# Performance work log

Hardware: AMD Instinct MI355X
Metric: run time of the kernel (lower is better)

The kernel has to match this reference:

```python
import jax, jax.numpy as jnp
import numpy as np

B, T_ENC, ENC, DEC, MEL = 32, 1024, 1024, 1024, 80


def setup_inputs() -> dict:
    key = jax.random.key(0)
    ks = jax.random.split(key, 10)
    s = lambda k, shape, sc=1.0: (jax.random.normal(k, shape, dtype=jnp.float32) * sc)
    return {
        "prev_mel_frame": s(ks[0], (B, MEL)),
        "encoder_outputs": s(ks[1], (B, T_ENC, ENC)),
        "h": s(ks[2], (B, DEC)),
        "c": s(ks[3], (B, DEC)),
        # AdditiveAttention learned scale vector (use_scale=True default)
        "attn_scale": s(ks[4], (ENC,), 0.05),
        # LSTMCell params: input dim = MEL + ENC, gates order i, f, c, o (Keras)
        "kernel": s(ks[5], (MEL + ENC, 4 * DEC), 0.02),
        "rec_kernel": s(ks[6], (DEC, 4 * DEC), 0.02),
        "bias": s(ks[7], (4 * DEC,), 0.02),
        # Dense projection to mel
        "proj_w": s(ks[8], (DEC, MEL), 0.02),
        "proj_b": s(ks[9], (MEL,), 0.02),
    }


def reference(prev_mel_frame, encoder_outputs, h, c,
              attn_scale, kernel, rec_kernel, bias, proj_w, proj_b):
    # Additive (Bahdanau) attention: scores[b,t] = sum_d scale_d * tanh(h[b,d] + enc[b,t,d])
    feat = jnp.tanh(h[:, None, :] + encoder_outputs)          # [B, T, D]
    scores = jnp.einsum("btd,d->bt", feat, attn_scale)         # [B, T]
    attn = jax.nn.softmax(scores, axis=-1)
    context = jnp.einsum("bt,btd->bd", attn, encoder_outputs)  # [B, ENC]

    # LSTMCell step on concat([prev_mel, context])
    x = jnp.concatenate([prev_mel_frame, context], axis=-1)    # [B, MEL+ENC]
    z = x @ kernel + h @ rec_kernel + bias                     # [B, 4*DEC]
    i, f, g, o = jnp.split(z, 4, axis=-1)
    i = jax.nn.sigmoid(i)
    f = jax.nn.sigmoid(f)
    o = jax.nn.sigmoid(o)
    c_new = f * c + i * jnp.tanh(g)
    h_new = o * jnp.tanh(c_new)

    mel_frame = h_new @ proj_w + proj_b                        # [B, MEL]
    return mel_frame, h_new, c_new
```

## Files before the change

kernel.cpp:

```cpp
#include <hip/hip_runtime.h>

#define BB 32
#define TT 1024
#define ENCD 1024
#define DECD 1024
#define MELD 80
#define KTOT (MELD + ENCD + DECD)
#define NZ (4 * DECD)
#define KCH 64
#define KC 34
#define NTT 32

__device__ float g_scores[BB * TT];
__device__ float g_cp[NTT * BB * ENCD];
__device__ float g_ctx[BB * ENCD];
__device__ float g_zp[KC * BB * NZ];
__device__ float g_hn[BB * DECD];

__device__ __forceinline__ float tanh_fast(float x) {
    return 1.f - __fdividef(2.f, __expf(2.f * x) + 1.f);
}
__device__ __forceinline__ float sigmoid_fast(float x) {
    return __fdividef(1.f, 1.f + __expf(-x));
}

__global__ __launch_bounds__(256) void k_scores(const float* __restrict__ enc,
                                                const float* __restrict__ h,
                                                const float* __restrict__ scale) {
    int w = blockIdx.x * 4 + (threadIdx.x >> 6);
    int lane = threadIdx.x & 63;
    int b = w >> 10;
    const float4* ep = (const float4*)(enc + (size_t)w * ENCD);
    const float4* hp = (const float4*)(h + (size_t)b * DECD);
    const float4* sp = (const float4*)scale;
    float sum = 0.f;
#pragma unroll
    for (int j = 0; j < 4; j++) {
        int i = lane + j * 64;
        float4 e = ep[i], hv = hp[i], s = sp[i];
        sum += s.x * tanh_fast(hv.x + e.x);
        sum += s.y * tanh_fast(hv.y + e.y);
        sum += s.z * tanh_fast(hv.z + e.z);
        sum += s.w * tanh_fast(hv.w + e.w);
    }
#pragma unroll
    for (int off = 32; off > 0; off >>= 1) sum += __shfl_down(sum, off, 64);
    if (lane == 0) g_scores[w] = sum;
}

__global__ __launch_bounds__(256) void k_context(const float* __restrict__ enc) {
    int b = blockIdx.x, tt = blockIdx.y, tid = threadIdx.x;
    __shared__ float red[4];
    __shared__ float la[32];
    float v[4];
#pragma unroll
    for (int i = 0; i < 4; i++) v[i] = g_scores[b * TT + tid + i * 256];
    float m = fmaxf(fmaxf(v[0], v[1]), fmaxf(v[2], v[3]));
#pragma unroll
    for (int off = 32; off > 0; off >>= 1) m = fmaxf(m, __shfl_down(m, off, 64));
    if ((tid & 63) == 0) red[tid >> 6] = m;
    __syncthreads();
    m = fmaxf(fmaxf(red[0], red[1]), fmaxf(red[2], red[3]));
    __syncthreads();
    float s = 0.f;
#pragma unroll
    for (int i = 0; i < 4; i++) s += __expf(v[i] - m);
#pragma unroll
    for (int off = 32; off > 0; off >>= 1) s += __shfl_down(s, off, 64);
    if ((tid & 63) == 0) red[tid >> 6] = s;
    __syncthreads();
    s = red[0] + red[1] + red[2] + red[3];
    float inv = __fdividef(1.f, s);
    if (tid < 32) la[tid] = __expf(g_scores[b * TT + tt * 32 + tid] - m) * inv;
    __syncthreads();

    const float4* ep = (const float4*)(enc + ((size_t)b * TT + tt * 32) * ENCD) + tid;
    float ax = 0.f, ay = 0.f, az = 0.f, aw = 0.f;
#pragma unroll 8
    for (int t = 0; t < 32; t++) {
        float4 e = ep[(size_t)t * (ENCD / 4)];
        float w = la[t];
        ax = fmaf(w, e.x, ax); ay = fmaf(w, e.y, ay);
        az = fmaf(w, e.z, az); aw = fmaf(w, e.w, aw);
    }
    float4 r; r.x = ax; r.y = ay; r.z = az; r.w = aw;
    ((float4*)g_cp)[((size_t)tt * BB + b) * (ENCD / 4) + tid] = r;
}

__global__ __launch_bounds__(256) void k_ctxsum() {
    int i = blockIdx.x * 256 + threadIdx.x;
    float a = 0.f;
#pragma unroll 8
    for (int tt = 0; tt < NTT; tt++) a += g_cp[tt * (BB * ENCD) + i];
    g_ctx[i] = a;
}

__global__ __launch_bounds__(256) void k_zmm(const float* __restrict__ pm,
                                             const float* __restrict__ h,
                                             const float* __restrict__ kern,
                                             const float* __restrict__ reck) {
    __shared__ float xs[KCH * 32];
    int jt = blockIdx.x & 15, kc = blockIdx.x >> 4;
    int k0 = kc * KCH;
    int kcount = min(KCH, KTOT - k0);
    int tid = threadIdx.x;
    for (int idx = tid; idx < kcount * 32; idx += 256) {
        int kk = idx >> 5, b = idx & 31;
        int k = k0 + kk;
        float v;
        if (k < MELD)             v = pm[b * MELD + k];
        else if (k < MELD + ENCD) v = g_ctx[b * ENCD + (k - MELD)];
        else                      v = h[b * DECD + (k - MELD - ENCD)];
        xs[idx] = v;
    }
    __syncthreads();
    int j = jt * 256 + tid;
    float acc[32];
#pragma unroll
    for (int b = 0; b < 32; b++) acc[b] = 0.f;
    for (int kk0 = 0; kk0 < kcount; kk0 += 8) {
        float w[8];
#pragma unroll
        for (int i = 0; i < 8; i++) {
            int k = k0 + kk0 + i;
            w[i] = (k < MELD + ENCD) ? kern[(size_t)k * NZ + j]
                                     : reck[(size_t)(k - MELD - ENCD) * NZ + j];
        }
#pragma unroll
        for (int i = 0; i < 8; i++) {
            const float* xr = xs + (kk0 + i) * 32;
#pragma unroll
            for (int b = 0; b < 32; b++) acc[b] = fmaf(xr[b], w[i], acc[b]);
        }
    }
#pragma unroll
    for (int b = 0; b < 32; b++) g_zp[((size_t)kc * BB + b) * NZ + j] = acc[b];
}

__global__ __launch_bounds__(256) void k_gates(const float* __restrict__ bias,
                                               const float* __restrict__ c,
                                               float* __restrict__ out) {
    __shared__ float sacc[4][4][64];
    int b = blockIdx.x >> 4, jq = blockIdx.x & 15;
    int jl = threadIdx.x & 63, grp = threadIdx.x >> 6;
    int j = jq * 64 + jl;
    int kc0 = grp * 9;
    int kc1 = min(kc0 + 9, KC);
    float zi = 0.f, zf = 0.f, zg = 0.f, zo = 0.f;
    for (int kc = kc0; kc < kc1; kc++) {
        const float* zp = g_zp + ((size_t)kc * BB + b) * NZ;
        zi += zp[j];
        zf += zp[1024 + j];
        zg += zp[2048 + j];
        zo += zp[3072 + j];
    }
    sacc[grp][0][jl] = zi; sacc[grp][1][jl] = zf;
    sacc[grp][2][jl] = zg; sacc[grp][3][jl] = zo;
    __syncthreads();
    if (grp == 0) {
        zi = sacc[0][0][jl] + sacc[1][0][jl] + sacc[2][0][jl] + sacc[3][0][jl] + bias[j];
        zf = sacc[0][1][jl] + sacc[1][1][jl] + sacc[2][1][jl] + sacc[3][1][jl] + bias[1024 + j];
        zg = sacc[0][2][jl] + sacc[1][2][jl] + sacc[2][2][jl] + sacc[3][2][jl] + bias[2048 + j];
        zo = sacc[0][3][jl] + sacc[1][3][jl] + sacc[2][3][jl] + sacc[3][3][jl] + bias[3072 + j];
        int idx = b * 1024 + j;
        float cn = sigmoid_fast(zf) * c[idx] + sigmoid_fast(zi) * tanh_fast(zg);
        float hn = sigmoid_fast(zo) * tanh_fast(cn);
        g_hn[idx] = hn;
        out[2560 + idx] = hn;
        out[35328 + idx] = cn;
    }
}

__global__ __launch_bounds__(256) void k_proj(const float* __restrict__ pw,
                                              const float* __restrict__ pb,
                                              float* __restrict__ out) {
    __shared__ float lh[1024];
    __shared__ float pacc[2][MELD];
    int b = blockIdx.x, tid = threadIdx.x;
    for (int i = tid; i < 1024; i += 256) lh[i] = g_hn[b * 1024 + i];
    __syncthreads();
    int m = tid & 127;
    int g = tid >> 7;
    if (m < MELD) {
        float acc = 0.f;
        int d0 = g * 512;
#pragma unroll 8
        for (int d = d0; d < d0 + 512; d++) acc = fmaf(lh[d], pw[d * MELD + m], acc);
        pacc[g][m] = acc;
    }
    __syncthreads();
    if (tid < MELD) out[b * MELD + tid] = pacc[0][tid] + pacc[1][tid] + pb[tid];
}

extern "C" void kernel_launch(void* const* d_in, const int* in_sizes, int n_in,
                              void* d_out, int out_size, void* d_ws, size_t ws_size,
                              hipStream_t stream) {
    const float* pm   = (const float*)d_in[0];
    const float* enc  = (const float*)d_in[1];
    const float* h    = (const float*)d_in[2];
    const float* c    = (const float*)d_in[3];
    const float* asc  = (const float*)d_in[4];
    const float* kern = (const float*)d_in[5];
    const float* reck = (const float*)d_in[6];
    const float* bias = (const float*)d_in[7];
    const float* pw   = (const float*)d_in[8];
    const float* pb   = (const float*)d_in[9];
    float* out = (float*)d_out;

    k_scores <<<8192, 256, 0, stream>>>(enc, h, asc);
    k_context<<<dim3(32, NTT), 256, 0, stream>>>(enc);
    k_ctxsum <<<128, 256, 0, stream>>>();
    k_zmm    <<<544, 256, 0, stream>>>(pm, h, kern, reck);
    k_gates  <<<512, 256, 0, stream>>>(bias, c, out);
    k_proj   <<<32, 256, 0, stream>>>(pw, pb, out);
}
```

Before: 299.5 us.

## Fuse attention scores, softmax and context into one online-softmax pass

```diff
diff --git a/kernel.cpp b/kernel.cpp
--- a/kernel.cpp
+++ b/kernel.cpp
@@ -11,8 +11,9 @@
 #define KC 34
 #define NTT 32
 
-__device__ float g_scores[BB * TT];
 __device__ float g_cp[NTT * BB * ENCD];
+__device__ float g_m[NTT * BB];
+__device__ float g_s[NTT * BB];
 __device__ float g_ctx[BB * ENCD];
 __device__ float g_zp[KC * BB * NZ];
 __device__ float g_hn[BB * DECD];
@@ -24,75 +25,122 @@
     return __fdividef(1.f, 1.f + __expf(-x));
 }
 
-__global__ __launch_bounds__(256) void k_scores(const float* __restrict__ enc,
-                                                const float* __restrict__ h,
-                                                const float* __restrict__ scale) {
-    int w = blockIdx.x * 4 + (threadIdx.x >> 6);
-    int lane = threadIdx.x & 63;
-    int b = w >> 10;
-    const float4* ep = (const float4*)(enc + (size_t)w * ENCD);
-    const float4* hp = (const float4*)(h + (size_t)b * DECD);
+__global__ __launch_bounds__(256) void k_attn(const float* __restrict__ enc,
+                                              const float* __restrict__ hst,
+                                              const float* __restrict__ scale) {
+    int b = blockIdx.x, tc = blockIdx.y;
+    int w = threadIdx.x >> 6, lane = threadIdx.x & 63;
+    const float4* hp = (const float4*)(hst + (size_t)b * DECD);
     const float4* sp = (const float4*)scale;
-    float sum = 0.f;
-#pragma unroll
-    for (int j = 0; j < 4; j++) {
-        int i = lane + j * 64;
-        float4 e = ep[i], hv = hp[i], s = sp[i];
-        sum += s.x * tanh_fast(hv.x + e.x);
-        sum += s.y * tanh_fast(hv.y + e.y);
-        sum += s.z * tanh_fast(hv.z + e.z);
-        sum += s.w * tanh_fast(hv.w + e.w);
-    }
-#pragma unroll
-    for (int off = 32; off > 0; off >>= 1) sum += __shfl_down(sum, off, 64);
-    if (lane == 0) g_scores[w] = sum;
-}
-
-__global__ __launch_bounds__(256) void k_context(const float* __restrict__ enc) {
-    int b = blockIdx.x, tt = blockIdx.y, tid = threadIdx.x;
-    __shared__ float red[4];
-    __shared__ float la[32];
-    float v[4];
-#pragma unroll
-    for (int i = 0; i < 4; i++) v[i] = g_scores[b * TT + tid + i * 256];
-    float m = fmaxf(fmaxf(v[0], v[1]), fmaxf(v[2], v[3]));
-#pragma unroll
-    for (int off = 32; off > 0; off >>= 1) m = fmaxf(m, __shfl_down(m, off, 64));
-    if ((tid & 63) == 0) red[tid >> 6] = m;
-    __syncthreads();
-    m = fmaxf(fmaxf(red[0], red[1]), fmaxf(red[2], red[3]));
-    __syncthreads();
-    float s = 0.f;
-#pragma unroll
-    for (int i = 0; i < 4; i++) s += __expf(v[i] - m);
-#pragma unroll
-    for (int off = 32; off > 0; off >>= 1) s += __shfl_down(s, off, 64);
-    if ((tid & 63) == 0) red[tid >> 6] = s;
-    __syncthreads();
-    s = red[0] + red[1] + red[2] + red[3];
-    float inv = __fdividef(1.f, s);
-    if (tid < 32) la[tid] = __expf(g_scores[b * TT + tt * 32 + tid] - m) * inv;
-    __syncthreads();
-
-    const float4* ep = (const float4*)(enc + ((size_t)b * TT + tt * 32) * ENCD) + tid;
+    float4 hr0 = hp[lane], hr1 = hp[lane + 64], hr2 = hp[lane + 128], hr3 = hp[lane + 192];
+    float4 sr0 = sp[lane], sr1 = sp[lane + 64], sr2 = sp[lane + 128], sr3 = sp[lane + 192];
+
+    float m = -1e30f, s = 0.f;
+    float4 c0 = {0.f, 0.f, 0.f, 0.f}, c1 = c0, c2 = c0, c3 = c0;
+
+    const float4* ep = (const float4*)(enc + ((size_t)b * TT + tc * 32 + w * 8) * ENCD) + lane;
+#pragma unroll 2
+    for (int t = 0; t < 8; t++) {
+        float4 e0 = ep[t * 256];
+        float4 e1 = ep[t * 256 + 64];
+        float4 e2 = ep[t * 256 + 128];
+        float4 e3 = ep[t * 256 + 192];
+        float sc = 0.f;
+        sc = fmaf(sr0.x, tanh_fast(hr0.x + e0.x), sc);
+        sc = fmaf(sr0.y, tanh_fast(hr0.y + e0.y), sc);
+        sc = fmaf(sr0.z, tanh_fast(hr0.z + e0.z), sc);
+        sc = fmaf(sr0.w, tanh_fast(hr0.w + e0.w), sc);
+        sc = fmaf(sr1.x, tanh_fast(hr1.x + e1.x), sc);
+        sc = fmaf(sr1.y, tanh_fast(hr1.y + e1.y), sc);
+        sc = fmaf(sr1.z, tanh_fast(hr1.z + e1.z), sc);
+        sc = fmaf(sr1.w, tanh_fast(hr1.w + e1.w), sc);
+        sc = fmaf(sr2.x, tanh_fast(hr2.x + e2.x), sc);
+        sc = fmaf(sr2.y, tanh_fast(hr2.y + e2.y), sc);
+        sc = fmaf(sr2.z, tanh_fast(hr2.z + e2.z), sc);
+        sc = fmaf(sr2.w, tanh_fast(hr2.w + e2.w), sc);
+        sc = fmaf(sr3.x, tanh_fast(hr3.x + e3.x), sc);
+        sc = fmaf(sr3.y, tanh_fast(hr3.y + e3.y), sc);
+        sc = fmaf(sr3.z, tanh_fast(hr3.z + e3.z), sc);
+        sc = fmaf(sr3.w, tanh_fast(hr3.w + e3.w), sc);
+#pragma unroll
+        for (int off = 32; off; off >>= 1) sc += __shfl_xor(sc, off, 64);
+        if (sc > m) {
+            float al = __expf(m - sc);
+            s = fmaf(s, al, 1.f);
+            c0.x = fmaf(c0.x, al, e0.x); c0.y = fmaf(c0.y, al, e0.y);
+            c0.z = fmaf(c0.z, al, e0.z); c0.w = fmaf(c0.w, al, e0.w);
+            c1.x = fmaf(c1.x, al, e1.x); c1.y = fmaf(c1.y, al, e1.y);
+            c1.z = fmaf(c1.z, al, e1.z); c1.w = fmaf(c1.w, al, e1.w);
+            c2.x = fmaf(c2.x, al, e2.x); c2.y = fmaf(c2.y, al, e2.y);
+            c2.z = fmaf(c2.z, al, e2.z); c2.w = fmaf(c2.w, al, e2.w);
+            c3.x = fmaf(c3.x, al, e3.x); c3.y = fmaf(c3.y, al, e3.y);
+            c3.z = fmaf(c3.z, al, e3.z); c3.w = fmaf(c3.w, al, e3.w);
+            m = sc;
+        } else {
+            float p = __expf(sc - m);
+            s += p;
+            c0.x = fmaf(p, e0.x, c0.x); c0.y = fmaf(p, e0.y, c0.y);
+            c0.z = fmaf(p, e0.z, c0.z); c0.w = fmaf(p, e0.w, c0.w);
+            c1.x = fmaf(p, e1.x, c1.x); c1.y = fmaf(p, e1.y, c1.y);
+            c1.z = fmaf(p, e1.z, c1.z); c1.w = fmaf(p, e1.w, c1.w);
+            c2.x = fmaf(p, e2.x, c2.x); c2.y = fmaf(p, e2.y, c2.y);
+            c2.z = fmaf(p, e2.z, c2.z); c2.w = fmaf(p, e2.w, c2.w);
+            c3.x = fmaf(p, e3.x, c3.x); c3.y = fmaf(p, e3.y, c3.y);
+            c3.z = fmaf(p, e3.z, c3.z); c3.w = fmaf(p, e3.w, c3.w);
+        }
+    }
+
+    __shared__ float lm[4], ls[4];
+    __shared__ float4 lctx[4][256];
+    if (lane == 0) { lm[w] = m; ls[w] = s; }
+    __syncthreads();
+    float M = fmaxf(fmaxf(lm[0], lm[1]), fmaxf(lm[2], lm[3]));
+    float S = ls[0] * __expf(lm[0] - M) + ls[1] * __expf(lm[1] - M) +
+              ls[2] * __expf(lm[2] - M) + ls[3] * __expf(lm[3] - M);
+    float be = __expf(m - M);
+    float4 o;
+    o.x = c0.x * be; o.y = c0.y * be; o.z = c0.z * be; o.w = c0.w * be;
+    lctx[w][lane] = o;
+    o.x = c1.x * be; o.y = c1.y * be; o.z = c1.z * be; o.w = c1.w * be;
+    lctx[w][lane + 64] = o;
+    o.x = c2.x * be; o.y = c2.y * be; o.z = c2.z * be; o.w = c2.w * be;
+    lctx[w][lane + 128] = o;
+    o.x = c3.x * be; o.y = c3.y * be; o.z = c3.z * be; o.w = c3.w * be;
+    lctx[w][lane + 192] = o;
+    __syncthreads();
+    int tid = threadIdx.x;
+    float4 a0 = lctx[0][tid], a1 = lctx[1][tid], a2 = lctx[2][tid], a3 = lctx[3][tid];
+    float4 r;
+    r.x = (a0.x + a1.x) + (a2.x + a3.x);
+    r.y = (a0.y + a1.y) + (a2.y + a3.y);
+    r.z = (a0.z + a1.z) + (a2.z + a3.z);
+    r.w = (a0.w + a1.w) + (a2.w + a3.w);
+    ((float4*)g_cp)[((size_t)tc * BB + b) * (ENCD / 4) + tid] = r;
+    if (tid == 0) { g_m[tc * BB + b] = M; g_s[tc * BB + b] = S; }
+}
+
+__global__ __launch_bounds__(256) void k_combine() {
+    __shared__ float wgt[NTT];
+    int b = blockIdx.x, tid = threadIdx.x;
+    float M = -1e30f;
+#pragma unroll
+    for (int tt = 0; tt < NTT; tt++) M = fmaxf(M, g_m[tt * BB + b]);
+    float S = 0.f;
+#pragma unroll
+    for (int tt = 0; tt < NTT; tt++) S += g_s[tt * BB + b] * __expf(g_m[tt * BB + b] - M);
+    if (tid < NTT) wgt[tid] = __expf(g_m[tid * BB + b] - M) * __fdividef(1.f, S);
+    __syncthreads();
+    const float4* cp = (const float4*)g_cp + (size_t)b * (ENCD / 4) + tid;
     float ax = 0.f, ay = 0.f, az = 0.f, aw = 0.f;
 #pragma unroll 8
-    for (int t = 0; t < 32; t++) {
-        float4 e = ep[(size_t)t * (ENCD / 4)];
-        float w = la[t];
-        ax = fmaf(w, e.x, ax); ay = fmaf(w, e.y, ay);
-        az = fmaf(w, e.z, az); aw = fmaf(w, e.w, aw);
+    for (int tt = 0; tt < NTT; tt++) {
+        float4 v = cp[(size_t)tt * (BB * ENCD / 4)];
+        float wv = wgt[tt];
+        ax = fmaf(wv, v.x, ax); ay = fmaf(wv, v.y, ay);
+        az = fmaf(wv, v.z, az); aw = fmaf(wv, v.w, aw);
     }
     float4 r; r.x = ax; r.y = ay; r.z = az; r.w = aw;
-    ((float4*)g_cp)[((size_t)tt * BB + b) * (ENCD / 4) + tid] = r;
-}
-
-__global__ __launch_bounds__(256) void k_ctxsum() {
-    int i = blockIdx.x * 256 + threadIdx.x;
-    float a = 0.f;
-#pragma unroll 8
-    for (int tt = 0; tt < NTT; tt++) a += g_cp[tt * (BB * ENCD) + i];
-    g_ctx[i] = a;
+    ((float4*)g_ctx)[b * (ENCD / 4) + tid] = r;
 }
 
 __global__ __launch_bounds__(256) void k_zmm(const float* __restrict__ pm,
@@ -207,9 +255,8 @@
     const float* pb   = (const float*)d_in[9];
     float* out = (float*)d_out;
 
-    k_scores <<<8192, 256, 0, stream>>>(enc, h, asc);
-    k_context<<<dim3(32, NTT), 256, 0, stream>>>(enc);
-    k_ctxsum <<<128, 256, 0, stream>>>();
+    k_attn   <<<dim3(32, NTT), 256, 0, stream>>>(enc, h, asc);
+    k_combine<<<32, 256, 0, stream>>>();
     k_zmm    <<<544, 256, 0, stream>>>(pm, h, kern, reck);
     k_gates  <<<512, 256, 0, stream>>>(bias, c, out);
     k_proj   <<<32, 256, 0, stream>>>(pw, pb, out);
```

Result: slower. 313.3 us (+4.6%).
